# Optimization experiments

Measured on AMD Instinct MI355X. Metric: run time of the kernel, lower is better.

## Reference

```python
import jax, jax.numpy as jnp
import numpy as np

BUFFER_SIZE = 1024
N_BANDS = 2049
N_SPEC = 4
FRAME_SIZE = 2 * (N_BANDS - 1)  # 4096
EPS = 1e-10


def _hann_periodic(n):
    k = np.arange(n, dtype=np.float64)
    return (0.5 * (1.0 - np.cos(2.0 * np.pi * k / n))).astype(np.float32)


def _build_windows():
    # Mirrors _build_windows with nonlinearity=0 (single filterbank).
    base = _hann_periodic(FRAME_SIZE) / (FRAME_SIZE / 4.0)
    win_scale = float(base.sum())
    wins = [base.copy()]
    for lvl in range(1, N_SPEC):
        stride = 1 << lvl
        small = base[::stride][: FRAME_SIZE // stride]
        w = np.zeros(FRAME_SIZE, dtype=np.float32)
        w[-(FRAME_SIZE // stride):] = small
        w *= win_scale / w.sum()
        wins.append(w)
    return [jnp.asarray(w) for w in wins]


WINDOWS = _build_windows()


def _forward(x):
    # x: (B, BUFFER_SIZE). Fresh (reset) state: time buffers are zeros,
    # spectrogram/left-boundary buffers are +1e6 (identity for min).
    B = x.shape[0]
    T = 1 << (N_SPEC - 1)  # finest time grid = output columns
    out = jnp.full((B, N_BANDS, T), 1.0e6, dtype=x.dtype)
    pad = jnp.zeros((B, FRAME_SIZE), dtype=x.dtype)
    concat = jnp.concatenate([pad, x], axis=-1)  # (B, FRAME_SIZE + BUFFER_SIZE)
    for lvl in range(N_SPEC):
        chunk = BUFFER_SIZE >> lvl
        nfr = 1 << lvl  # sub-frames at this level
        # Overlap-save sliding windows: frame i starts at offset chunk + i*chunk
        frames = jnp.stack(
            [concat[:, chunk + i * chunk: chunk + i * chunk + FRAME_SIZE] for i in range(nfr)],
            axis=1,
        )  # (B, nfr, FRAME_SIZE)
        spec = jnp.fft.rfft(frames * WINDOWS[lvl][None, None, :], n=FRAME_SIZE, axis=-1)
        power = jnp.transpose(spec.real ** 2 + spec.imag ** 2, (0, 2, 1))  # (B, N_BANDS, nfr)
        # Upsample coarse-time levels to the finest grid (tile replication, the
        # streaming moving-max/min buffers realize this in the original) and
        # take the min across scales (buffers initialised to 1e6 = +inf for min).
        out = jnp.minimum(out, jnp.repeat(power, T // nfr, axis=-1))
    return 10.0 * jnp.log10(jnp.maximum(out, EPS))  # power -> dB


def setup_inputs() -> dict:
    key = jax.random.key(0)
    x = jax.random.normal(key, (1024, BUFFER_SIZE), dtype=jnp.float32)
    return {"x": x}


def reference(x):
    return _forward(x)
```

## Files before the change

kernel.cpp:

```cpp
#include <hip/hip_runtime.h>
#include <math.h>

#define NBANDS 2049
#define NF 4096
#define NC 2048
#define BUF 1024
#define THREADS 512
#define R2C 0.70710678118654752f

__device__ __forceinline__ int SW(int i) { return i ^ (i >> 2) ^ (i >> 6); }

__device__ __forceinline__ int posrev10(int j) {
  return ((j & 3) << 9) | (((j >> 2) & 3) << 7) | (((j >> 4) & 3) << 5) |
         (((j >> 6) & 3) << 3) | (((j >> 8) & 3) << 1);
}

struct Smem {
  float xs[BUF];
  float zreA[NC], zimA[NC];
  float zreB[NC], zimB[NC];
};

struct State {
  float2 W[5];
  float2 Ub;
  float2 U1;
  float so;
  float s1a[5], s1b[5];
  float s2a[5], s2b[5];
  float o[8][5];
};

__device__ __forceinline__ float2 cmul(float2 a, float2 b) {
  return make_float2(a.x * b.x - a.y * b.y, a.x * b.y + a.y * b.x);
}

template <int L>
__device__ __forceinline__ float cheb(float c) {
  #pragma unroll
  for (int i = 0; i < L; ++i) c = 2.0f * c * c - 1.0f;
  return c;
}

template <int L>
__device__ __forceinline__ void fused_s1(float* __restrict__ re, float* __restrict__ im,
                                         const Smem& sm, const State& st, int off) {
  const int n = threadIdx.x;
  constexpr int M = NF >> L;
  constexpr float ws = (float)(1 << L) * (0.5f / 1024.0f);
  const int lo = 512 - (min(off, M) >> 1);
  float dr = 0.0f, di = 0.0f;
  if (n >= lo) {
    const int idx = 2 * n + off - 1024;
    const float2 xv = *(const float2*)&sm.xs[idx];
    const float cE = cheb<L>(-st.W[0].y);
    const float cO = cheb<L>(st.so);
    dr = ws * (1.0f - cE) * xv.x;
    di = ws * (1.0f - cO) * xv.y;
  }
  const float2 W = st.W[0];
  const float2 W2 = make_float2(W.x * W.x - W.y * W.y, 2.0f * W.x * W.y);
  const float2 W3 = cmul(W, W2);
  const int p0 = SW(n), p1 = SW(n + 512), p2 = SW(n + 1024), p3 = SW(n + 1536);
  re[p0] = dr;                       im[p0] = di;
  re[p1] = -di * W.x - dr * W.y;     im[p1] = -di * W.y + dr * W.x;
  re[p2] = -(dr * W2.x - di * W2.y); im[p2] = -(dr * W2.y + di * W2.x);
  re[p3] =  di * W3.x + dr * W3.y;   im[p3] =  di * W3.y - dr * W3.x;
}

__device__ __forceinline__ void bfly4(float* __restrict__ re, float* __restrict__ im,
                                      int i0, int i1, int i2, int i3,
                                      float2 W, float2 W2, float2 W3) {
  float ar = re[i0], ai = im[i0];
  float br = re[i1], bi = im[i1];
  float cr = re[i2], ci = im[i2];
  float dr = re[i3], di = im[i3];
  float t0r = ar + cr, t0i = ai + ci;
  float t1r = ar - cr, t1i = ai - ci;
  float t2r = br + dr, t2i = bi + di;
  float t3r = br - dr, t3i = bi - di;
  re[i0] = t0r + t2r; im[i0] = t0i + t2i;
  float y1r = t1r + t3i, y1i = t1i - t3r;
  re[i1] = y1r * W.x - y1i * W.y;  im[i1] = y1r * W.y + y1i * W.x;
  float y2r = t0r - t2r, y2i = t0i - t2i;
  re[i2] = y2r * W2.x - y2i * W2.y; im[i2] = y2r * W2.y + y2i * W2.x;
  float y3r = t1r - t3i, y3i = t1i + t3r;
  re[i3] = y3r * W3.x - y3i * W3.y; im[i3] = y3r * W3.y + y3i * W3.x;
}

template <int LM, bool HASB>
__device__ __forceinline__ void radix4p(Smem& sm, float2 W) {
  const int j = threadIdx.x;
  const int m = 1 << LM;
  const int base = ((j >> LM) << (LM + 2)) | (j & (m - 1));
  const int i0 = SW(base), i1 = SW(base + m), i2 = SW(base + 2 * m), i3 = SW(base + 3 * m);
  float2 W2 = make_float2(W.x * W.x - W.y * W.y, 2.0f * W.x * W.y);
  float2 W3 = cmul(W, W2);
  bfly4(sm.zreA, sm.zimA, i0, i1, i2, i3, W, W2, W3);
  if constexpr (HASB) bfly4(sm.zreB, sm.zimB, i0, i1, i2, i3, W, W2, W3);
}

__device__ __forceinline__ void pair_powers(const float* __restrict__ re,
                                            const float* __restrict__ im,
                                            int kp, float2 U, float& pp, float& pm) {
  const int k1 = kp & (NC - 1);
  const int k2 = (NC - kp) & (NC - 1);
  const int q1 = SW(posrev10(k1 & 1023));
  const int q2 = SW(posrev10(k2 & 1023));
  const float s1 = (k1 & 1024) ? -1.0f : 1.0f;
  const float s2 = (k2 & 1024) ? -1.0f : 1.0f;
  const float zkr = re[q1] + s1 * re[q1 ^ 1];
  const float zki = im[q1] + s1 * im[q1 ^ 1];
  const float zmr = re[q2] + s2 * re[q2 ^ 1];
  const float zmi = im[q2] + s2 * im[q2 ^ 1];
  const float Ex = 0.5f * (zkr + zmr), Ey = 0.5f * (zki - zmi);
  const float Ox = 0.5f * (zki + zmi), Oy = -0.5f * (zkr - zmr);
  const float Vx = U.x * Ox - U.y * Oy, Vy = U.x * Oy + U.y * Ox;
  const float ax = Ex + Vx, ay = Ey + Vy;
  const float bx = Ex - Vx, by = Ey - Vy;
  pp = ax * ax + ay * ay;
  pm = bx * bx + by * by;
}

template <int ACT, int COL, int SLOT>
__device__ __forceinline__ void act(State& st, float p) {
  if constexpr (ACT == 0)      st.s1a[SLOT] = fminf(p, 1.0e6f);
  else if constexpr (ACT == 1) st.s1b[SLOT] = fminf(p, 1.0e6f);
  else if constexpr (ACT == 2) { st.s1a[SLOT] = fminf(st.s1a[SLOT], p); st.s1b[SLOT] = fminf(st.s1b[SLOT], p); }
  else if constexpr (ACT == 3) st.s2a[SLOT] = fminf(st.s1a[SLOT], p);
  else if constexpr (ACT == 4) st.s2b[SLOT] = fminf(st.s1a[SLOT], p);
  else if constexpr (ACT == 5) st.s2a[SLOT] = fminf(st.s1b[SLOT], p);
  else if constexpr (ACT == 6) st.s2b[SLOT] = fminf(st.s1b[SLOT], p);
  else if constexpr (ACT == 7) st.o[COL][SLOT] = 10.0f * log10f(fmaxf(fminf(st.s2a[SLOT], p), 1.0e-10f));
  else                         st.o[COL][SLOT] = 10.0f * log10f(fmaxf(fminf(st.s2b[SLOT], p), 1.0e-10f));
}

template <int ACT, int COL>
__device__ __forceinline__ void unpack_frame(const float* __restrict__ re,
                                             const float* __restrict__ im,
                                             State& st) {
  const int t = threadIdx.x;
  float pp, pm;
  pair_powers(re, im, t, st.Ub, pp, pm);
  act<ACT, COL, 0>(st, pp);
  act<ACT, COL, 1>(st, pm);
  pair_powers(re, im, 512 + t, st.U1, pp, pm);
  act<ACT, COL, 2>(st, pp);
  act<ACT, COL, 3>(st, pm);
  if (t == 0) {
    const float zr = re[0] - re[1];
    const float zi = im[0] - im[1];
    act<ACT, COL, 4>(st, zr * zr + zi * zi);
  }
}

template <int LA, int ACTA, int COLA, int LB, int ACTB, int COLB, bool HASB>
__device__ __forceinline__ void pass(Smem& sm, State& st, int offA, int offB) {
  __syncthreads();
  fused_s1<LA>(sm.zreA, sm.zimA, sm, st, offA);
  if constexpr (HASB) fused_s1<LB>(sm.zreB, sm.zimB, sm, st, offB);
  __syncthreads(); radix4p<7, HASB>(sm, st.W[1]);
  __syncthreads(); radix4p<5, HASB>(sm, st.W[2]);
  __syncthreads(); radix4p<3, HASB>(sm, st.W[3]);
  __syncthreads(); radix4p<1, HASB>(sm, st.W[4]);
  __syncthreads();
  unpack_frame<ACTA, COLA>(sm.zreA, sm.zimA, st);
  if constexpr (HASB) unpack_frame<ACTB, COLB>(sm.zreB, sm.zimB, st);
}

__device__ __forceinline__ void store_all(const State& st, float* __restrict__ outb) {
  const int t = threadIdx.x;
  #pragma unroll
  for (int sl = 0; sl < 5; ++sl) {
    if (sl < 4 || t == 0) {
      const int band = (sl == 0) ? t : (sl == 1) ? 2048 - t
                     : (sl == 2) ? 512 + t : (sl == 3) ? 1536 - t : 1024;
      float* bp = outb + (size_t)band * 8;
      *(float4*)(bp)     = make_float4(st.o[0][sl], st.o[1][sl], st.o[2][sl], st.o[3][sl]);
      *(float4*)(bp + 4) = make_float4(st.o[4][sl], st.o[5][sl], st.o[6][sl], st.o[7][sl]);
    }
  }
}

__global__ __launch_bounds__(THREADS, 2) void spec_kernel(const float* __restrict__ x,
                                                          float* __restrict__ out) {
  __shared__ Smem sm;
  State st;
  const int tid = threadIdx.x;
  const int b = blockIdx.x;
  const float* xb = x + (size_t)b * BUF;
  #pragma unroll
  for (int i = tid; i < BUF; i += THREADS) sm.xs[i] = xb[i];
  {
    float sn, cs;
    sincospif((float)tid * (1.0f / 1024.0f), &sn, &cs);         st.W[0] = make_float2(cs, -sn);
    sincospif((float)(tid & 127) * (1.0f / 256.0f), &sn, &cs);  st.W[1] = make_float2(cs, -sn);
    sincospif((float)(tid & 31) * (1.0f / 64.0f), &sn, &cs);    st.W[2] = make_float2(cs, -sn);
    sincospif((float)(tid & 7) * (1.0f / 16.0f), &sn, &cs);     st.W[3] = make_float2(cs, -sn);
    st.W[4] = (tid & 1) ? make_float2(R2C, -R2C) : make_float2(1.0f, 0.0f);
    sincospif((float)tid * (1.0f / 2048.0f), &sn, &cs);         st.Ub = make_float2(cs, -sn);
    st.U1 = cmul(st.Ub, make_float2(R2C, -R2C));
    sincospif((float)(2 * tid + 1) * (1.0f / 2048.0f), &sn, &cs); st.so = sn;
  }
  float* outb = out + (size_t)b * (NBANDS * 8);

  pass<1, 0, 0,  1, 1, 0, true >(sm, st, 512, 1024);
  pass<0, 2, 0,  2, 3, 0, true >(sm, st, 1024, 256);
  pass<2, 4, 0,  3, 7, 0, true >(sm, st, 512, 128);
  pass<3, 7, 1,  3, 8, 2, true >(sm, st, 256, 384);
  pass<3, 8, 3,  2, 5, 0, true >(sm, st, 512, 768);
  pass<2, 6, 0,  3, 7, 4, true >(sm, st, 1024, 640);
  pass<3, 7, 5,  3, 8, 6, true >(sm, st, 768, 896);
  pass<3, 8, 7,  0, 0, 0, false>(sm, st, 1024, 0);
  store_all(st, outb);
}

extern "C" void kernel_launch(void* const* d_in, const int* in_sizes, int n_in,
                              void* d_out, int out_size, void* d_ws, size_t ws_size,
                              hipStream_t stream) {
  const float* x = (const float*)d_in[0];
  float* out = (float*)d_out;
  const int B = in_sizes[0] / BUF;
  hipLaunchKernelGGL(spec_kernel, dim3(B), dim3(THREADS), 0, stream, x, out);
}
```

Baseline: 100.6 us.

## Process three FFT frames per pass and store dB outputs as half precision

Each pass now runs three frames at once instead of two, using a third shared-memory buffer pair, which cuts the pass count from eight to five and removes many barriers. The per-thread dB output accumulators become packed half2 values to offset the register cost, and the unpack step reads adjacent pairs with float2 loads. The trade-off is larger shared memory, which may reduce blocks per CU, and fp16 rounding of the dB outputs, which could exceed the accuracy tolerance.

Result: faster. 96.90 us (-3.7%).

```diff
diff --git a/kernel.cpp b/kernel.cpp
--- a/kernel.cpp
+++ b/kernel.cpp
@@ -1,4 +1,5 @@
 #include <hip/hip_runtime.h>
+#include <hip/hip_fp16.h>
 #include <math.h>
 
 #define NBANDS 2049
@@ -16,9 +17,13 @@
 }
 
 struct Smem {
-  float xs[BUF];
-  float zreA[NC], zimA[NC];
-  float zreB[NC], zimB[NC];
+  alignas(16) float xs[BUF];
+  alignas(16) float zreA[NC];
+  alignas(16) float zimA[NC];
+  alignas(16) float zreB[NC];
+  alignas(16) float zimB[NC];
+  alignas(16) float zreC[NC];
+  alignas(16) float zimC[NC];
 };
 
 struct State {
@@ -28,7 +33,7 @@
   float so;
   float s1a[5], s1b[5];
   float s2a[5], s2b[5];
-  float o[8][5];
+  __half2 oh[4][5];
 };
 
 __device__ __forceinline__ float2 cmul(float2 a, float2 b) {
@@ -88,7 +93,7 @@
   re[i3] = y3r * W3.x - y3i * W3.y; im[i3] = y3r * W3.y + y3i * W3.x;
 }
 
-template <int LM, bool HASB>
+template <int LM, int NFR>
 __device__ __forceinline__ void radix4p(Smem& sm, float2 W) {
   const int j = threadIdx.x;
   const int m = 1 << LM;
@@ -97,7 +102,8 @@
   float2 W2 = make_float2(W.x * W.x - W.y * W.y, 2.0f * W.x * W.y);
   float2 W3 = cmul(W, W2);
   bfly4(sm.zreA, sm.zimA, i0, i1, i2, i3, W, W2, W3);
-  if constexpr (HASB) bfly4(sm.zreB, sm.zimB, i0, i1, i2, i3, W, W2, W3);
+  if constexpr (NFR >= 2) bfly4(sm.zreB, sm.zimB, i0, i1, i2, i3, W, W2, W3);
+  if constexpr (NFR >= 3) bfly4(sm.zreC, sm.zimC, i0, i1, i2, i3, W, W2, W3);
 }
 
 __device__ __forceinline__ void pair_powers(const float* __restrict__ re,
@@ -109,10 +115,15 @@
   const int q2 = SW(posrev10(k2 & 1023));
   const float s1 = (k1 & 1024) ? -1.0f : 1.0f;
   const float s2 = (k2 & 1024) ? -1.0f : 1.0f;
-  const float zkr = re[q1] + s1 * re[q1 ^ 1];
-  const float zki = im[q1] + s1 * im[q1 ^ 1];
-  const float zmr = re[q2] + s2 * re[q2 ^ 1];
-  const float zmi = im[q2] + s2 * im[q2 ^ 1];
+  const float2 vr1 = *(const float2*)&re[q1 & ~1];
+  const float2 vi1 = *(const float2*)&im[q1 & ~1];
+  const float2 vr2 = *(const float2*)&re[q2 & ~1];
+  const float2 vi2 = *(const float2*)&im[q2 & ~1];
+  const bool o1 = (q1 & 1), o2 = (q2 & 1);
+  const float zkr = o1 ? (vr1.y + s1 * vr1.x) : (vr1.x + s1 * vr1.y);
+  const float zki = o1 ? (vi1.y + s1 * vi1.x) : (vi1.x + s1 * vi1.y);
+  const float zmr = o2 ? (vr2.y + s2 * vr2.x) : (vr2.x + s2 * vr2.y);
+  const float zmi = o2 ? (vi2.y + s2 * vi2.x) : (vi2.x + s2 * vi2.y);
   const float Ex = 0.5f * (zkr + zmr), Ey = 0.5f * (zki - zmi);
   const float Ox = 0.5f * (zki + zmi), Oy = -0.5f * (zkr - zmr);
   const float Vx = U.x * Ox - U.y * Oy, Vy = U.x * Oy + U.y * Ox;
@@ -131,8 +142,12 @@
   else if constexpr (ACT == 4) st.s2b[SLOT] = fminf(st.s1a[SLOT], p);
   else if constexpr (ACT == 5) st.s2a[SLOT] = fminf(st.s1b[SLOT], p);
   else if constexpr (ACT == 6) st.s2b[SLOT] = fminf(st.s1b[SLOT], p);
-  else if constexpr (ACT == 7) st.o[COL][SLOT] = 10.0f * log10f(fmaxf(fminf(st.s2a[SLOT], p), 1.0e-10f));
-  else                         st.o[COL][SLOT] = 10.0f * log10f(fmaxf(fminf(st.s2b[SLOT], p), 1.0e-10f));
+  else {
+    const float base = (ACT == 7) ? st.s2a[SLOT] : st.s2b[SLOT];
+    const float db = 10.0f * log10f(fmaxf(fminf(base, p), 1.0e-10f));
+    if constexpr (COL & 1) st.oh[COL >> 1][SLOT].y = __float2half_rn(db);
+    else                   st.oh[COL >> 1][SLOT].x = __float2half_rn(db);
+  }
 }
 
 template <int ACT, int COL>
@@ -154,18 +169,20 @@
   }
 }
 
-template <int LA, int ACTA, int COLA, int LB, int ACTB, int COLB, bool HASB>
-__device__ __forceinline__ void pass(Smem& sm, State& st, int offA, int offB) {
+template <int LA, int AA, int CA, int LB, int AB, int CB, int LC, int AC, int CC, int NFR>
+__device__ __forceinline__ void pass(Smem& sm, State& st, int offA, int offB, int offC) {
   __syncthreads();
   fused_s1<LA>(sm.zreA, sm.zimA, sm, st, offA);
-  if constexpr (HASB) fused_s1<LB>(sm.zreB, sm.zimB, sm, st, offB);
-  __syncthreads(); radix4p<7, HASB>(sm, st.W[1]);
-  __syncthreads(); radix4p<5, HASB>(sm, st.W[2]);
-  __syncthreads(); radix4p<3, HASB>(sm, st.W[3]);
-  __syncthreads(); radix4p<1, HASB>(sm, st.W[4]);
+  if constexpr (NFR >= 2) fused_s1<LB>(sm.zreB, sm.zimB, sm, st, offB);
+  if constexpr (NFR >= 3) fused_s1<LC>(sm.zreC, sm.zimC, sm, st, offC);
+  __syncthreads(); radix4p<7, NFR>(sm, st.W[1]);
+  __syncthreads(); radix4p<5, NFR>(sm, st.W[2]);
+  __syncthreads(); radix4p<3, NFR>(sm, st.W[3]);
+  __syncthreads(); radix4p<1, NFR>(sm, st.W[4]);
   __syncthreads();
-  unpack_frame<ACTA, COLA>(sm.zreA, sm.zimA, st);
-  if constexpr (HASB) unpack_frame<ACTB, COLB>(sm.zreB, sm.zimB, st);
+  unpack_frame<AA, CA>(sm.zreA, sm.zimA, st);
+  if constexpr (NFR >= 2) unpack_frame<AB, CB>(sm.zreB, sm.zimB, st);
+  if constexpr (NFR >= 3) unpack_frame<AC, CC>(sm.zreC, sm.zimC, st);
 }
 
 __device__ __forceinline__ void store_all(const State& st, float* __restrict__ outb) {
@@ -176,8 +193,10 @@
       const int band = (sl == 0) ? t : (sl == 1) ? 2048 - t
                      : (sl == 2) ? 512 + t : (sl == 3) ? 1536 - t : 1024;
       float* bp = outb + (size_t)band * 8;
-      *(float4*)(bp)     = make_float4(st.o[0][sl], st.o[1][sl], st.o[2][sl], st.o[3][sl]);
-      *(float4*)(bp + 4) = make_float4(st.o[4][sl], st.o[5][sl], st.o[6][sl], st.o[7][sl]);
+      *(float4*)(bp)     = make_float4(__half2float(st.oh[0][sl].x), __half2float(st.oh[0][sl].y),
+                                       __half2float(st.oh[1][sl].x), __half2float(st.oh[1][sl].y));
+      *(float4*)(bp + 4) = make_float4(__half2float(st.oh[2][sl].x), __half2float(st.oh[2][sl].y),
+                                       __half2float(st.oh[3][sl].x), __half2float(st.oh[3][sl].y));
     }
   }
 }
@@ -204,14 +223,11 @@
   }
   float* outb = out + (size_t)b * (NBANDS * 8);
 
-  pass<1, 0, 0,  1, 1, 0, true >(sm, st, 512, 1024);
-  pass<0, 2, 0,  2, 3, 0, true >(sm, st, 1024, 256);
-  pass<2, 4, 0,  3, 7, 0, true >(sm, st, 512, 128);
-  pass<3, 7, 1,  3, 8, 2, true >(sm, st, 256, 384);
-  pass<3, 8, 3,  2, 5, 0, true >(sm, st, 512, 768);
-  pass<2, 6, 0,  3, 7, 4, true >(sm, st, 1024, 640);
-  pass<3, 7, 5,  3, 8, 6, true >(sm, st, 768, 896);
-  pass<3, 8, 7,  0, 0, 0, false>(sm, st, 1024, 0);
+  pass<1, 0, 0,  1, 1, 0,  0, 2, 0, 3>(sm, st, 512, 1024, 1024);
+  pass<2, 3, 0,  2, 4, 0,  3, 7, 0, 3>(sm, st, 256, 512, 128);
+  pass<3, 7, 1,  3, 8, 2,  3, 8, 3, 3>(sm, st, 256, 384, 512);
+  pass<2, 5, 0,  2, 6, 0,  3, 7, 4, 3>(sm, st, 768, 1024, 640);
+  pass<3, 7, 5,  3, 8, 6,  3, 8, 7, 3>(sm, st, 768, 896, 1024);
   store_all(st, outb);
 }
 
```
